# Performance work log

Measured on AMD Instinct MI355X. Metric: run time of the kernel, lower is better.

The kernel has to match this reference:

```python
import jax, jax.numpy as jnp
import numpy as np

N, E, IN_DIM, HID, L = 50000, 800000, 64, 64, 3
EDGE_DIM = 2 * HID + 2  # src_h | dst_h | edge_feat


def setup_inputs() -> dict:
    key = jax.random.key(0)
    ks = jax.random.split(key, 32)
    s = 0.05
    inp = {
        "h": jax.random.normal(ks[0], (N, IN_DIM), jnp.float32),
        "e": jax.random.normal(ks[1], (E, 2), jnp.float32),
        "src": jax.random.randint(ks[2], (E,), 0, N),
        "dst": jax.random.randint(ks[3], (E,), 0, N),
        # input embedding
        "emb_W": jax.random.normal(ks[4], (IN_DIM, HID), jnp.float32) * s,
        "emb_b": jnp.zeros((HID,), jnp.float32),
        # per-GIN-layer params (stacked over L)
        "eps": jnp.zeros((L,), jnp.float32),  # learn_eps init 0
        "mlp_W1": jax.random.normal(ks[5], (L, HID, HID), jnp.float32) * s,
        "mlp_b1": jnp.zeros((L, HID), jnp.float32),
        "mlp_bn_s": jnp.ones((L, HID), jnp.float32),   # eval-mode BN folded: x*s+sh
        "mlp_bn_sh": jnp.zeros((L, HID), jnp.float32),
        "mlp_W2": jax.random.normal(ks[6], (L, HID, HID), jnp.float32) * s,
        "mlp_b2": jnp.zeros((L, HID), jnp.float32),
        "apply_bn_s": jnp.ones((L, HID), jnp.float32),
        "apply_bn_sh": jnp.zeros((L, HID), jnp.float32),
        "gin_bn_s": jnp.ones((L, HID), jnp.float32),
        "gin_bn_sh": jnp.zeros((L, HID), jnp.float32),
        # prediction heads (L+1 of them)
        "pred_W1": jax.random.normal(ks[7], (L + 1, EDGE_DIM, HID), jnp.float32) * s,
        "pred_b1": jnp.zeros((L + 1, HID), jnp.float32),
        "pred_W2": jax.random.normal(ks[8], (L + 1, HID, 1), jnp.float32) * s,
        "pred_b2": jnp.zeros((L + 1, 1), jnp.float32),
    }
    return inp


def reference(h, e, src, dst, emb_W, emb_b, eps,
              mlp_W1, mlp_b1, mlp_bn_s, mlp_bn_sh, mlp_W2, mlp_b2,
              apply_bn_s, apply_bn_sh, gin_bn_s, gin_bn_sh,
              pred_W1, pred_b1, pred_W2, pred_b2):
    n = h.shape[0]
    bn = lambda x, sc, sh: x * sc + sh  # eval-mode batchnorm (folded scale/shift)

    h = h @ emb_W + emb_b  # [N, HID]

    def edge_feat(hh):
        # gather node features onto edges: [E, 2*HID+2]
        return jnp.concatenate([hh[src], hh[dst], e], axis=1)

    def pred(ef, i):
        z = jax.nn.relu(ef @ pred_W1[i] + pred_b1[i])
        return z @ pred_W2[i] + pred_b2[i]  # [E, 1]

    score = pred(edge_feat(h), 0)
    for i in range(L):
        h_in = h
        # GIN sum aggregation: copy src features, sum at dst
        neigh = jax.ops.segment_sum(h[src], dst, num_segments=n)
        x = (1.0 + eps[i]) * h + neigh
        # MLP: Linear -> BN -> ReLU -> Linear
        x = jax.nn.relu(bn(x @ mlp_W1[i] + mlp_b1[i], mlp_bn_s[i], mlp_bn_sh[i]))
        x = x @ mlp_W2[i] + mlp_b2[i]
        # ApplyNodeFunc: BN -> ReLU
        x = jax.nn.relu(bn(x, apply_bn_s[i], apply_bn_sh[i]))
        # GINLayer post: BN -> ReLU -> residual (dropout=0 in eval)
        x = jax.nn.relu(bn(x, gin_bn_s[i], gin_bn_sh[i]))
        h = h_in + x
        score = score + pred(edge_feat(h), i + 1)
    return jax.nn.relu(score)
```

## Files before the change

### kernel.cpp

```cpp
#include <hip/hip_runtime.h>

typedef unsigned short ushort_t;
typedef unsigned int uint_t;

static __device__ __forceinline__ ushort_t f2bf(float f) {
    uint_t u = __float_as_uint(f);
    uint_t r = (u + 0x7FFFu + ((u >> 16) & 1u)) >> 16;
    return (ushort_t)r;
}
static __device__ __forceinline__ float bf2f(ushort_t u) {
    return __uint_as_float(((uint_t)u) << 16);
}
static __device__ __forceinline__ float bf2f_lo(uint_t u) {
    return __uint_as_float(u << 16);
}
static __device__ __forceinline__ float bf2f_hi(uint_t u) {
    return __uint_as_float(u & 0xffff0000u);
}
static __device__ __forceinline__ uint_t pack2(float lo, float hi) {
    return (uint_t)f2bf(lo) | ((uint_t)f2bf(hi) << 16);
}

static __device__ __forceinline__ float edge_p2(
    uint_t ax, uint_t ay, float4 brow, float ex, float ey,
    float4 wc0, float4 wc1, float4 w2v)
{
    float z0 = bf2f_lo(ax) + brow.x + ex*wc0.x + ey*wc1.x; z0 = fmaxf(z0, 0.f);
    float z1 = bf2f_hi(ax) + brow.y + ex*wc0.y + ey*wc1.y; z1 = fmaxf(z1, 0.f);
    float z2 = bf2f_lo(ay) + brow.z + ex*wc0.z + ey*wc1.z; z2 = fmaxf(z2, 0.f);
    float z3 = bf2f_hi(ay) + brow.w + ex*wc0.w + ey*wc1.w; z3 = fmaxf(z3, 0.f);
    return z0*w2v.x + z1*w2v.y + z2*w2v.z + z3*w2v.w;
}

#define RED16(p) { p += __shfl_xor(p,1); p += __shfl_xor(p,2); \
                   p += __shfl_xor(p,4); p += __shfl_xor(p,8); }

__global__ __launch_bounds__(256) void k_count(
    const int* __restrict__ dst, int* __restrict__ deg, int E)
{
    int e = blockIdx.x * 256 + threadIdx.x;
    if (e < E) atomicAdd(&deg[dst[e]], 1);
}

__global__ __launch_bounds__(1024) void k_scanA(
    const int* __restrict__ deg, int* __restrict__ partial,
    int* __restrict__ bsum, int N)
{
    __shared__ int wsum[16];
    int tid = threadIdx.x, lane = tid & 63, wid = tid >> 6;
    int idx = blockIdx.x * 1024 + tid;
    int v = (idx < N) ? deg[idx] : 0;
    int x = v;
#pragma unroll
    for (int o = 1; o < 64; o <<= 1) {
        int t = __shfl_up(x, o, 64);
        if (lane >= o) x += t;
    }
    if (lane == 63) wsum[wid] = x;
    __syncthreads();
    if (wid == 0) {
        int s = (lane < 16) ? wsum[lane] : 0;
#pragma unroll
        for (int o = 1; o < 16; o <<= 1) {
            int t = __shfl_up(s, o, 64);
            if (lane >= o) s += t;
        }
        if (lane < 16) wsum[lane] = s;
    }
    __syncthreads();
    int woff = (wid > 0) ? wsum[wid - 1] : 0;
    if (idx < N) partial[idx] = woff + x - v;
    if (tid == 0) bsum[blockIdx.x] = wsum[15];
}

__global__ __launch_bounds__(256) void k_scanB(
    int* __restrict__ bsum, int nb, int* __restrict__ totalp)
{
    __shared__ int s[256];
    int tid = threadIdx.x;
    int v = (tid < nb) ? bsum[tid] : 0;
    s[tid] = v;
    __syncthreads();
#pragma unroll
    for (int off = 1; off < 256; off <<= 1) {
        int t = (tid >= off) ? s[tid - off] : 0;
        __syncthreads();
        s[tid] += t;
        __syncthreads();
    }
    if (tid < nb) bsum[tid] = s[tid] - v;
    if (tid == 0) totalp[0] = s[255];
}

__global__ __launch_bounds__(256) void k_scanC(
    int* __restrict__ offsets, const int* __restrict__ bsum,
    int* __restrict__ cursor, int N)
{
    int idx = blockIdx.x * 256 + threadIdx.x;
    if (idx >= N) return;
    int o = offsets[idx] + bsum[idx >> 10];
    offsets[idx] = o;
    cursor[idx] = o;
}

__global__ __launch_bounds__(256) void k_fill(
    const int* __restrict__ src, const int* __restrict__ dst,
    const float* __restrict__ ep, int* __restrict__ cursor,
    int4* __restrict__ entries, int E)
{
    int ei = blockIdx.x * 256 + threadIdx.x;
    if (ei >= E) return;
    int pos = atomicAdd(&cursor[dst[ei]], 1);
    float2 ev = *(const float2*)(ep + 2 * (size_t)ei);
    entries[pos] = make_int4(src[ei], ei, __float_as_int(ev.x), __float_as_int(ev.y));
}

static __device__ __forceinline__ int deg_bucket(int d) {
    return d >= 63 ? 0 : (63 - d);
}

__global__ __launch_bounds__(256) void k_bcount(
    const int* __restrict__ offsets, int* __restrict__ bcnt, int N)
{
    __shared__ int hist[64];
    int tid = threadIdx.x;
    if (tid < 64) hist[tid] = 0;
    __syncthreads();
    int idx = blockIdx.x * 256 + tid;
    if (idx < N) {
        int d = offsets[idx + 1] - offsets[idx];
        atomicAdd(&hist[deg_bucket(d)], 1);
    }
    __syncthreads();
    if (tid < 64 && hist[tid]) atomicAdd(&bcnt[tid], hist[tid]);
}

__global__ __launch_bounds__(64) void k_bscan(
    int* __restrict__ bcnt, int* __restrict__ bcur)
{
    int lane = threadIdx.x;
    int v = bcnt[lane];
    int x = v;
#pragma unroll
    for (int o = 1; o < 64; o <<= 1) {
        int t = __shfl_up(x, o, 64);
        if (lane >= o) x += t;
    }
    bcur[lane] = x - v;
}

__global__ __launch_bounds__(256) void k_bfill(
    const int* __restrict__ offsets, int* __restrict__ bcur,
    int* __restrict__ perm, int N)
{
    __shared__ int hist[64];
    __shared__ int lbase[64];
    int tid = threadIdx.x;
    if (tid < 64) hist[tid] = 0;
    __syncthreads();
    int idx = blockIdx.x * 256 + tid;
    int b = 0, rank = 0;
    bool valid = (idx < N);
    if (valid) {
        int d = offsets[idx + 1] - offsets[idx];
        b = deg_bucket(d);
        rank = atomicAdd(&hist[b], 1);
    }
    __syncthreads();
    if (tid < 64) lbase[tid] = hist[tid] ? atomicAdd(&bcur[tid], hist[tid]) : 0;
    __syncthreads();
    if (valid) perm[lbase[b] + rank] = idx;
}

template <int WRITE>
static __device__ __forceinline__ void epi_tables16(
    float (*xs)[68], int row16, int li, int r, float4 o,
    const float* __restrict__ WAn, const float* __restrict__ bAn,
    const float* __restrict__ WBn,
    ushort_t* __restrict__ tab_out, ushort_t* __restrict__ B_out)
{
    xs[row16][4*li+0] = o.x; xs[row16][4*li+1] = o.y;
    xs[row16][4*li+2] = o.z; xs[row16][4*li+3] = o.w;
    float4 aA = *(const float4*)(bAn + 4 * li);
    float4 aB = make_float4(0.f, 0.f, 0.f, 0.f);
#pragma unroll
    for (int k = 0; k < 64; k++) {
        float xk = xs[row16][k];
        float4 wa = *(const float4*)(WAn + k * 64 + 4 * li);
        float4 wb = *(const float4*)(WBn + k * 64 + 4 * li);
        aA.x += xk * wa.x; aA.y += xk * wa.y; aA.z += xk * wa.z; aA.w += xk * wa.w;
        aB.x += xk * wb.x; aB.y += xk * wb.y; aB.z += xk * wb.z; aB.w += xk * wb.w;
    }
    if (WRITE == 1) {
        int4 cw;
        cw.x = (int)pack2(aA.x, aA.y);
        cw.y = (int)pack2(aA.z, aA.w);
        cw.z = (int)pack2(o.x, o.y);
        cw.w = (int)pack2(o.z, o.w);
        *(int4*)(tab_out + (size_t)r * 128 + li * 8) = cw;
    } else {
        ushort4 oa;
        oa.x = f2bf(aA.x); oa.y = f2bf(aA.y); oa.z = f2bf(aA.z); oa.w = f2bf(aA.w);
        *(ushort4*)(tab_out + (size_t)r * 64 + 4 * li) = oa;
    }
    ushort4 ob;
    ob.x = f2bf(aB.x); ob.y = f2bf(aB.y); ob.z = f2bf(aB.z); ob.w = f2bf(aB.w);
    *(ushort4*)(B_out + (size_t)r * 64 + 4 * li) = ob;
}

__global__ __launch_bounds__(256) void k_embed_ab(
    const float* __restrict__ in, const float* __restrict__ W,
    const float* __restrict__ bias, float* __restrict__ hout,
    const float* __restrict__ WA, const float* __restrict__ bA,
    const float* __restrict__ WB,
    ushort_t* __restrict__ comb_out, ushort_t* __restrict__ B_out, int N)
{
    __shared__ float xs[16][68];
    const int row16 = threadIdx.x >> 4;
    const int li    = threadIdx.x & 15;
    const int r     = blockIdx.x * 16 + row16;
    if (r >= N) return;
    float4 x4 = *(const float4*)(in + (size_t)r * 64 + 4 * li);
    xs[row16][4*li+0] = x4.x; xs[row16][4*li+1] = x4.y;
    xs[row16][4*li+2] = x4.z; xs[row16][4*li+3] = x4.w;
    float4 acc = *(const float4*)(bias + 4 * li);
#pragma unroll
    for (int k = 0; k < 64; k++) {
        float xk = xs[row16][k];
        float4 wv = *(const float4*)(W + k * 64 + 4 * li);
        acc.x += xk * wv.x; acc.y += xk * wv.y;
        acc.z += xk * wv.z; acc.w += xk * wv.w;
    }
    *(float4*)(hout + (size_t)r * 64 + 4 * li) = acc;
    epi_tables16<1>(xs, row16, li, r, acc, WA, bA, WB, comb_out, B_out);
}

__global__ __launch_bounds__(256) void k_tables(
    const float* __restrict__ h,
    const float* __restrict__ WA, const float* __restrict__ bA,
    const float* __restrict__ WB,
    ushort_t* __restrict__ comb_out, ushort_t* __restrict__ B_out, int N)
{
    __shared__ float xs[16][68];
    const int row16 = threadIdx.x >> 4;
    const int li    = threadIdx.x & 15;
    const int r     = blockIdx.x * 16 + row16;
    if (r >= N) return;
    float4 o = *(const float4*)(h + (size_t)r * 64 + 4 * li);
    epi_tables16<1>(xs, row16, li, r, o, WA, bA, WB, comb_out, B_out);
}

template <int MODE, int EPI>
__global__ __launch_bounds__(256) void k_fused(
    const float* __restrict__ h, float* __restrict__ hout,
    const ushort_t* __restrict__ comb, const ushort_t* __restrict__ Bm,
    const int4* __restrict__ entries, const int* __restrict__ offsets,
    const int* __restrict__ perm,
    float* __restrict__ score_csr,
    const float* __restrict__ Wc, const float* __restrict__ W2v,
    const float* __restrict__ b2p, const float* __restrict__ epsp,
    const float* __restrict__ W1, const float* __restrict__ b1,
    const float* __restrict__ s1, const float* __restrict__ sh1,
    const float* __restrict__ W2, const float* __restrict__ b2,
    const float* __restrict__ as_, const float* __restrict__ ash,
    const float* __restrict__ gs, const float* __restrict__ gsh,
    const float* __restrict__ WAn, const float* __restrict__ bAn,
    const float* __restrict__ WBn,
    ushort_t* __restrict__ tab_out, ushort_t* __restrict__ B_out, int N)
{
    __shared__ float xs[16][68];
    __shared__ float ts[16][68];
    const int row16 = threadIdx.x >> 4;
    const int li    = threadIdx.x & 15;
    const int idx   = blockIdx.x * 16 + row16;
    if (idx >= N) return;
    const int r = perm[idx];

    const float4 wc0 = *(const float4*)(Wc + li*4);
    const float4 wc1 = *(const float4*)(Wc + 64 + li*4);
    const float4 w2v = *(const float4*)(W2v + li*4);
    const float bb2 = b2p[0];
    ushort4 bu = *(const ushort4*)(Bm + (size_t)r * 64 + li*4);
    const float4 brow = make_float4(bf2f(bu.x), bf2f(bu.y), bf2f(bu.z), bf2f(bu.w));

    const int beg = offsets[r], end = offsets[r + 1];
    float4 acc = make_float4(0.f, 0.f, 0.f, 0.f);

    for (int k = beg; k < end; k += 8) {
        int4 ee[8];
#pragma unroll
        for (int j = 0; j < 8; j++) {
            int kj = k + j; kj = kj < end ? kj : end - 1;
            ee[j] = entries[kj];
        }
        int4 cc[8];
#pragma unroll
        for (int j = 0; j < 8; j++)
            cc[j] = *(const int4*)(comb + (size_t)ee[j].x * 128 + li * 8);
#pragma unroll
        for (int j = 0; j < 8; j++) {
            const bool ok = (k + j < end);
            uint_t hz = ok ? (uint_t)cc[j].z : 0u;
            uint_t hw = ok ? (uint_t)cc[j].w : 0u;
            acc.x += bf2f_lo(hz); acc.y += bf2f_hi(hz);
            acc.z += bf2f_lo(hw); acc.w += bf2f_hi(hw);
        }
#pragma unroll
        for (int j = 0; j < 8; j++) {
            float p = edge_p2((uint_t)cc[j].x, (uint_t)cc[j].y, brow,
                              __int_as_float(ee[j].z), __int_as_float(ee[j].w),
                              wc0, wc1, w2v);
            RED16(p)
            if (li == 0 && (k + j < end)) {
                if (MODE == 0) score_csr[k + j] = p + bb2;
                else           score_csr[k + j] += p + bb2;
            }
        }
    }

    const float epsv = 1.0f + epsp[0];
    float4 hv = *(const float4*)(h + (size_t)r * 64 + 4 * li);
    xs[row16][4*li+0] = epsv * hv.x + acc.x;
    xs[row16][4*li+1] = epsv * hv.y + acc.y;
    xs[row16][4*li+2] = epsv * hv.z + acc.z;
    xs[row16][4*li+3] = epsv * hv.w + acc.w;

    float4 t = *(const float4*)(b1 + 4 * li);
#pragma unroll
    for (int kk = 0; kk < 64; kk++) {
        float xk = xs[row16][kk];
        float4 wv = *(const float4*)(W1 + kk * 64 + 4 * li);
        t.x += xk * wv.x; t.y += xk * wv.y; t.z += xk * wv.z; t.w += xk * wv.w;
    }
    {
        float4 sc = *(const float4*)(s1 + 4 * li);
        float4 sh = *(const float4*)(sh1 + 4 * li);
        t.x = fmaxf(t.x * sc.x + sh.x, 0.f);
        t.y = fmaxf(t.y * sc.y + sh.y, 0.f);
        t.z = fmaxf(t.z * sc.z + sh.z, 0.f);
        t.w = fmaxf(t.w * sc.w + sh.w, 0.f);
    }
    ts[row16][4*li+0] = t.x; ts[row16][4*li+1] = t.y;
    ts[row16][4*li+2] = t.z; ts[row16][4*li+3] = t.w;

    float4 u = *(const float4*)(b2 + 4 * li);
#pragma unroll
    for (int kk = 0; kk < 64; kk++) {
        float tk = ts[row16][kk];
        float4 wv = *(const float4*)(W2 + kk * 64 + 4 * li);
        u.x += tk * wv.x; u.y += tk * wv.y; u.z += tk * wv.z; u.w += tk * wv.w;
    }
    {
        float4 sc = *(const float4*)(as_ + 4 * li);
        float4 sh = *(const float4*)(ash + 4 * li);
        u.x = fmaxf(u.x * sc.x + sh.x, 0.f);
        u.y = fmaxf(u.y * sc.y + sh.y, 0.f);
        u.z = fmaxf(u.z * sc.z + sh.z, 0.f);
        u.w = fmaxf(u.w * sc.w + sh.w, 0.f);
        sc = *(const float4*)(gs + 4 * li);
        sh = *(const float4*)(gsh + 4 * li);
        u.x = fmaxf(u.x * sc.x + sh.x, 0.f);
        u.y = fmaxf(u.y * sc.y + sh.y, 0.f);
        u.z = fmaxf(u.z * sc.z + sh.z, 0.f);
        u.w = fmaxf(u.w * sc.w + sh.w, 0.f);
    }
    float4 o = make_float4(hv.x + u.x, hv.y + u.y, hv.z + u.z, hv.w + u.w);
    *(float4*)(hout + (size_t)r * 64 + 4 * li) = o;

    if (EPI == 1)
        epi_tables16<1>(xs, row16, li, r, o, WAn, bAn, WBn, tab_out, B_out);
    else if (EPI == 2)
        epi_tables16<2>(xs, row16, li, r, o, WAn, bAn, WBn, tab_out, B_out);
}

template <int COMPACT>
__global__ __launch_bounds__(256) void k_head(
    const ushort_t* __restrict__ Atab,
    const ushort_t* __restrict__ Bm,
    const int4* __restrict__ entries, const int* __restrict__ offsets,
    const int* __restrict__ perm,
    const float* __restrict__ score_csr, float* __restrict__ score_out,
    const float* __restrict__ Wc, const float* __restrict__ W2v,
    const float* __restrict__ b2p, int N)
{
    const int row16 = threadIdx.x >> 4;
    const int li    = threadIdx.x & 15;
    const int idx   = blockIdx.x * 16 + row16;
    if (idx >= N) return;
    const int r = perm[idx];

    const float4 wc0 = *(const float4*)(Wc + li*4);
    const float4 wc1 = *(const float4*)(Wc + 64 + li*4);
    const float4 w2v = *(const float4*)(W2v + li*4);
    const float bb2 = b2p[0];
    ushort4 bu = *(const ushort4*)(Bm + (size_t)r * 64 + li*4);
    const float4 brow = make_float4(bf2f(bu.x), bf2f(bu.y), bf2f(bu.z), bf2f(bu.w));

    const int beg = offsets[r], end = offsets[r + 1];

    for (int k = beg; k < end; k += 8) {
        int4 ee[8];
#pragma unroll
        for (int j = 0; j < 8; j++) {
            int kj = k + j; kj = kj < end ? kj : end - 1;
            ee[j] = entries[kj];
        }
        uint_t ax[8], ay[8];
#pragma unroll
        for (int j = 0; j < 8; j++) {
            if (COMPACT) {
                ushort4 a = *(const ushort4*)(Atab + (size_t)ee[j].x * 64 + li * 4);
                ax[j] = (uint_t)a.x | ((uint_t)a.y << 16);
                ay[j] = (uint_t)a.z | ((uint_t)a.w << 16);
            } else {
                int2 d = *(const int2*)(Atab + (size_t)ee[j].x * 128 + li * 8);
                ax[j] = (uint_t)d.x; ay[j] = (uint_t)d.y;
            }
        }
#pragma unroll
        for (int j = 0; j < 8; j++) {
            float p = edge_p2(ax[j], ay[j], brow,
                              __int_as_float(ee[j].z), __int_as_float(ee[j].w),
                              wc0, wc1, w2v);
            RED16(p)
            if (li == 0 && (k + j < end))
                score_out[ee[j].y] = fmaxf(score_csr[k + j] + p + bb2, 0.f);
        }
    }
}

extern "C" void kernel_launch(void* const* d_in, const int* in_sizes, int n_in,
                              void* d_out, int out_size, void* d_ws, size_t ws_size,
                              hipStream_t stream) {
    const float* h_in  = (const float*)d_in[0];
    const float* e     = (const float*)d_in[1];
    const int*   src   = (const int*)d_in[2];
    const int*   dst   = (const int*)d_in[3];
    const float* emb_W = (const float*)d_in[4];
    const float* emb_b = (const float*)d_in[5];
    const float* eps   = (const float*)d_in[6];
    const float* mW1   = (const float*)d_in[7];
    const float* mb1   = (const float*)d_in[8];
    const float* mbs   = (const float*)d_in[9];
    const float* mbsh  = (const float*)d_in[10];
    const float* mW2   = (const float*)d_in[11];
    const float* mb2   = (const float*)d_in[12];
    const float* as_   = (const float*)d_in[13];
    const float* ash   = (const float*)d_in[14];
    const float* gs    = (const float*)d_in[15];
    const float* gsh   = (const float*)d_in[16];
    const float* pW1   = (const float*)d_in[17];
    const float* pb1   = (const float*)d_in[18];
    const float* pW2   = (const float*)d_in[19];
    const float* pb2   = (const float*)d_in[20];

    const int N  = in_sizes[0] / 64;
    const int E  = in_sizes[2];
    const int Lr = in_sizes[6];
    const size_t nrow = (size_t)N * 64;

    float* score = (float*)d_out;

    char* wp = (char*)d_ws;
    auto take = [&](size_t b) -> char* {
        char* p = wp; wp += (b + 255) & ~(size_t)255; return p;
    };
    float*    h0        = (float*)take(nrow * 4);
    float*    h1        = (float*)take(nrow * 4);
    ushort_t* comb0     = (ushort_t*)take(nrow * 4);
    ushort_t* B0        = (ushort_t*)take(nrow * 2);
    int4*     entries   = (int4*)take((size_t)E * 16);
    float*    score_csr = (float*)take((size_t)E * 4);
    int*      offsets   = (int*)take((size_t)(N + 1) * 4);
    int*      cursor    = (int*)take((size_t)N * 4);
    int*      bsum      = (int*)take(1024);
    int*      perm      = (int*)take((size_t)N * 4);
    int*      bcnt      = (int*)take(64 * 4);
    int*      bcur      = (int*)take(64 * 4);
    ushort_t* comb1     = (ushort_t*)take(nrow * 4);
    ushort_t* B1        = (ushort_t*)take(nrow * 2);
    ushort_t* Afin      = (ushort_t*)take(nrow * 2);
    size_t need_epi = (size_t)(wp - (char*)d_ws);

    const bool use_epi = ws_size >= need_epi;

    const int rowBlocks = (N + 15) / 16;
    const int edgeGrid  = (E + 255) / 256;
    const int nb        = (N + 1023) / 1024;

    hipMemsetAsync(cursor, 0, (size_t)N * sizeof(int), stream);
    k_count<<<edgeGrid, 256, 0, stream>>>(dst, cursor, E);
    k_scanA<<<nb, 1024, 0, stream>>>(cursor, offsets, bsum, N);
    k_scanB<<<1, 256, 0, stream>>>(bsum, nb, offsets + N);
    k_scanC<<<(N + 255) / 256, 256, 0, stream>>>(offsets, bsum, cursor, N);
    k_fill<<<edgeGrid, 256, 0, stream>>>(src, dst, e, cursor, entries, E);

    hipMemsetAsync(bcnt, 0, 64 * sizeof(int), stream);
    k_bcount<<<(N + 255) / 256, 256, 0, stream>>>(offsets, bcnt, N);
    k_bscan<<<1, 64, 0, stream>>>(bcnt, bcur);
    k_bfill<<<(N + 255) / 256, 256, 0, stream>>>(offsets, bcur, perm, N);

    k_embed_ab<<<rowBlocks, 256, 0, stream>>>(
        h_in, emb_W, emb_b, h0, pW1, pb1, pW1 + 64 * 64, comb0, B0, N);

    float* hcur = h0;       float* hnext = h1;
    ushort_t* Ccur = comb0; ushort_t* Cnxt = use_epi ? comb1 : comb0;
    ushort_t* Bcur = B0;    ushort_t* Bnxt = use_epi ? B1 : B0;

    for (int i = 0; i < Lr; i++) {
        const float* pw  = pW1 + (size_t)i * 130 * 64;
        const float* Wc  = pw + 128 * 64;
        const float* w2  = pW2 + (size_t)i * 64;
        const float* b2  = pb2 + i;
        const float* pwn = pW1 + (size_t)(i + 1) * 130 * 64;
        const float* gW1 = mW1 + (size_t)i * 64 * 64;
        const float* gW2 = mW2 + (size_t)i * 64 * 64;
        const bool last = (i == Lr - 1);

        if (use_epi) {
            ushort_t* tout = last ? Afin : Cnxt;
            if (i == 0 && !last)
                k_fused<0,1><<<rowBlocks, 256, 0, stream>>>(
                    hcur, hnext, Ccur, Bcur, entries, offsets, perm, score_csr,
                    Wc, w2, b2, eps + i,
                    gW1, mb1 + i*64, mbs + i*64, mbsh + i*64, gW2, mb2 + i*64,
                    as_ + i*64, ash + i*64, gs + i*64, gsh + i*64,
                    pwn, pb1 + (i+1)*64, pwn + 64*64, tout, Bnxt, N);
            else if (i == 0 && last)
                k_fused<0,2><<<rowBlocks, 256, 0, stream>>>(
                    hcur, hnext, Ccur, Bcur, entries, offsets, perm, score_csr,
                    Wc, w2, b2, eps + i,
                    gW1, mb1 + i*64, mbs + i*64, mbsh + i*64, gW2, mb2 + i*64,
                    as_ + i*64, ash + i*64, gs + i*64, gsh + i*64,
                    pwn, pb1 + (i+1)*64, pwn + 64*64, tout, Bnxt, N);
            else if (!last)
                k_fused<1,1><<<rowBlocks, 256, 0, stream>>>(
                    hcur, hnext, Ccur, Bcur, entries, offsets, perm, score_csr,
                    Wc, w2, b2, eps + i,
                    gW1, mb1 + i*64, mbs + i*64, mbsh + i*64, gW2, mb2 + i*64,
                    as_ + i*64, ash + i*64, gs + i*64, gsh + i*64,
                    pwn, pb1 + (i+1)*64, pwn + 64*64, tout, Bnxt, N);
            else
                k_fused<1,2><<<rowBlocks, 256, 0, stream>>>(
                    hcur, hnext, Ccur, Bcur, entries, offsets, perm, score_csr,
                    Wc, w2, b2, eps + i,
                    gW1, mb1 + i*64, mbs + i*64, mbsh + i*64, gW2, mb2 + i*64,
                    as_ + i*64, ash + i*64, gs + i*64, gsh + i*64,
                    pwn, pb1 + (i+1)*64, pwn + 64*64, tout, Bnxt, N);
            { ushort_t* t = Ccur; Ccur = Cnxt; Cnxt = t; }
            { ushort_t* t = Bcur; Bcur = Bnxt; Bnxt = t; }
        } else {
            if (i == 0)
                k_fused<0,0><<<rowBlocks, 256, 0, stream>>>(
                    hcur, hnext, Ccur, Bcur, entries, offsets, perm, score_csr,
                    Wc, w2, b2, eps + i,
                    gW1, mb1 + i*64, mbs + i*64, mbsh + i*64, gW2, mb2 + i*64,
                    as_ + i*64, ash + i*64, gs + i*64, gsh + i*64,
                    nullptr, nullptr, nullptr, nullptr, nullptr, N);
            else
                k_fused<1,0><<<rowBlocks, 256, 0, stream>>>(
                    hcur, hnext, Ccur, Bcur, entries, offsets, perm, score_csr,
                    Wc, w2, b2, eps + i,
                    gW1, mb1 + i*64, mbs + i*64, mbsh + i*64, gW2, mb2 + i*64,
                    as_ + i*64, ash + i*64, gs + i*64, gsh + i*64,
                    nullptr, nullptr, nullptr, nullptr, nullptr, N);
            k_tables<<<rowBlocks, 256, 0, stream>>>(
                hnext, pwn, pb1 + (i+1)*64, pwn + 64*64, Ccur, Bcur, N);
        }
        { float* t = hcur; hcur = hnext; hnext = t; }
    }

    {
        const float* pw = pW1 + (size_t)Lr * 130 * 64;
        const float* Wc = pw + 128 * 64;
        const float* w2 = pW2 + (size_t)Lr * 64;
        const float* b2 = pb2 + Lr;
        if (use_epi)
            k_head<1><<<rowBlocks, 256, 0, stream>>>(
                Afin, Bcur, entries, offsets, perm, score_csr, score,
                Wc, w2, b2, N);
        else
            k_head<0><<<rowBlocks, 256, 0, stream>>>(
                Ccur, Bcur, entries, offsets, perm, score_csr, score,
                Wc, w2, b2, N);
    }
}
```

Measured before the change: 612.9 us.

## Process two nodes per 16-lane group and fold degree histogram into scan

The fused layer kernel now has each 16-lane group handle two degree-sorted nodes, interleaving their edge gathers four at a time so more independent memory loads are in flight. The per-node MLP and table epilogue move into a helper that runs twice, and the second shared buffer is dropped by reusing xs. The degree-bucket histogram is computed inside k_scanA, which removes the separate k_bcount launch, and the head kernel's edge loop switches from 8-wide clamped batches to 4-wide batches with a scalar tail. The trade-off is more registers per thread and half as many blocks, which could lower occupancy.

After: 1.432 ms. 134% more time.

```diff
diff --git a/kernel.cpp b/kernel.cpp
--- a/kernel.cpp
+++ b/kernel.cpp
@@ -42,14 +42,22 @@
     if (e < E) atomicAdd(&deg[dst[e]], 1);
 }
 
+static __device__ __forceinline__ int deg_bucket(int d) {
+    return d >= 63 ? 0 : (63 - d);
+}
+
 __global__ __launch_bounds__(1024) void k_scanA(
     const int* __restrict__ deg, int* __restrict__ partial,
-    int* __restrict__ bsum, int N)
+    int* __restrict__ bsum, int* __restrict__ bcnt, int N)
 {
     __shared__ int wsum[16];
+    __shared__ int hist[64];
     int tid = threadIdx.x, lane = tid & 63, wid = tid >> 6;
+    if (tid < 64) hist[tid] = 0;
+    __syncthreads();
     int idx = blockIdx.x * 1024 + tid;
     int v = (idx < N) ? deg[idx] : 0;
+    if (idx < N) atomicAdd(&hist[deg_bucket(v)], 1);
     int x = v;
 #pragma unroll
     for (int o = 1; o < 64; o <<= 1) {
@@ -71,6 +79,8 @@
     int woff = (wid > 0) ? wsum[wid - 1] : 0;
     if (idx < N) partial[idx] = woff + x - v;
     if (tid == 0) bsum[blockIdx.x] = wsum[15];
+    __syncthreads();
+    if (tid < 64 && hist[tid]) atomicAdd(&bcnt[tid], hist[tid]);
 }
 
 __global__ __launch_bounds__(256) void k_scanB(
@@ -113,26 +123,6 @@
     int pos = atomicAdd(&cursor[dst[ei]], 1);
     float2 ev = *(const float2*)(ep + 2 * (size_t)ei);
     entries[pos] = make_int4(src[ei], ei, __float_as_int(ev.x), __float_as_int(ev.y));
-}
-
-static __device__ __forceinline__ int deg_bucket(int d) {
-    return d >= 63 ? 0 : (63 - d);
-}
-
-__global__ __launch_bounds__(256) void k_bcount(
-    const int* __restrict__ offsets, int* __restrict__ bcnt, int N)
-{
-    __shared__ int hist[64];
-    int tid = threadIdx.x;
-    if (tid < 64) hist[tid] = 0;
-    __syncthreads();
-    int idx = blockIdx.x * 256 + tid;
-    if (idx < N) {
-        int d = offsets[idx + 1] - offsets[idx];
-        atomicAdd(&hist[deg_bucket(d)], 1);
-    }
-    __syncthreads();
-    if (tid < 64 && hist[tid]) atomicAdd(&bcnt[tid], hist[tid]);
 }
 
 __global__ __launch_bounds__(64) void k_bscan(
@@ -174,18 +164,18 @@
 
 template <int WRITE>
 static __device__ __forceinline__ void epi_tables16(
-    float (*xs)[68], int row16, int li, int r, float4 o,
+    float (*xs)[68], int row, int li, int r, float4 o,
     const float* __restrict__ WAn, const float* __restrict__ bAn,
     const float* __restrict__ WBn,
     ushort_t* __restrict__ tab_out, ushort_t* __restrict__ B_out)
 {
-    xs[row16][4*li+0] = o.x; xs[row16][4*li+1] = o.y;
-    xs[row16][4*li+2] = o.z; xs[row16][4*li+3] = o.w;
+    xs[row][4*li+0] = o.x; xs[row][4*li+1] = o.y;
+    xs[row][4*li+2] = o.z; xs[row][4*li+3] = o.w;
     float4 aA = *(const float4*)(bAn + 4 * li);
     float4 aB = make_float4(0.f, 0.f, 0.f, 0.f);
 #pragma unroll
     for (int k = 0; k < 64; k++) {
-        float xk = xs[row16][k];
+        float xk = xs[row][k];
         float4 wa = *(const float4*)(WAn + k * 64 + 4 * li);
         float4 wb = *(const float4*)(WBn + k * 64 + 4 * li);
         aA.x += xk * wa.x; aA.y += xk * wa.y; aA.z += xk * wa.z; aA.w += xk * wa.w;
@@ -208,6 +198,72 @@
     *(ushort4*)(B_out + (size_t)r * 64 + 4 * li) = ob;
 }
 
+template <int EPI>
+static __device__ __forceinline__ void node_mlp(
+    float (*xs)[68], int row, int li, int r, float4 acc, float epsv,
+    const float* __restrict__ h, float* __restrict__ hout,
+    const float* __restrict__ W1, const float* __restrict__ b1,
+    const float* __restrict__ s1, const float* __restrict__ sh1,
+    const float* __restrict__ W2, const float* __restrict__ b2,
+    const float* __restrict__ as_, const float* __restrict__ ash,
+    const float* __restrict__ gs, const float* __restrict__ gsh,
+    const float* __restrict__ WAn, const float* __restrict__ bAn,
+    const float* __restrict__ WBn,
+    ushort_t* __restrict__ tab_out, ushort_t* __restrict__ B_out)
+{
+    float4 hv = *(const float4*)(h + (size_t)r * 64 + 4 * li);
+    xs[row][4*li+0] = epsv * hv.x + acc.x;
+    xs[row][4*li+1] = epsv * hv.y + acc.y;
+    xs[row][4*li+2] = epsv * hv.z + acc.z;
+    xs[row][4*li+3] = epsv * hv.w + acc.w;
+
+    float4 t = *(const float4*)(b1 + 4 * li);
+#pragma unroll
+    for (int kk = 0; kk < 64; kk++) {
+        float xk = xs[row][kk];
+        float4 wv = *(const float4*)(W1 + kk * 64 + 4 * li);
+        t.x += xk * wv.x; t.y += xk * wv.y; t.z += xk * wv.z; t.w += xk * wv.w;
+    }
+    {
+        float4 sc = *(const float4*)(s1 + 4 * li);
+        float4 sh = *(const float4*)(sh1 + 4 * li);
+        t.x = fmaxf(t.x * sc.x + sh.x, 0.f);
+        t.y = fmaxf(t.y * sc.y + sh.y, 0.f);
+        t.z = fmaxf(t.z * sc.z + sh.z, 0.f);
+        t.w = fmaxf(t.w * sc.w + sh.w, 0.f);
+    }
+    xs[row][4*li+0] = t.x; xs[row][4*li+1] = t.y;
+    xs[row][4*li+2] = t.z; xs[row][4*li+3] = t.w;
+
+    float4 u = *(const float4*)(b2 + 4 * li);
+#pragma unroll
+    for (int kk = 0; kk < 64; kk++) {
+        float tk = xs[row][kk];
+        float4 wv = *(const float4*)(W2 + kk * 64 + 4 * li);
+        u.x += tk * wv.x; u.y += tk * wv.y; u.z += tk * wv.z; u.w += tk * wv.w;
+    }
+    {
+        float4 sc = *(const float4*)(as_ + 4 * li);
+        float4 sh = *(const float4*)(ash + 4 * li);
+        u.x = fmaxf(u.x * sc.x + sh.x, 0.f);
+        u.y = fmaxf(u.y * sc.y + sh.y, 0.f);
+        u.z = fmaxf(u.z * sc.z + sh.z, 0.f);
+        u.w = fmaxf(u.w * sc.w + sh.w, 0.f);
+        sc = *(const float4*)(gs + 4 * li);
+        sh = *(const float4*)(gsh + 4 * li);
+        u.x = fmaxf(u.x * sc.x + sh.x, 0.f);
+        u.y = fmaxf(u.y * sc.y + sh.y, 0.f);
+        u.z = fmaxf(u.z * sc.z + sh.z, 0.f);
+        u.w = fmaxf(u.w * sc.w + sh.w, 0.f);
+    }
+    float4 o = make_float4(hv.x + u.x, hv.y + u.y, hv.z + u.z, hv.w + u.w);
+    *(float4*)(hout + (size_t)r * 64 + 4 * li) = o;
+    if (EPI == 1)
+        epi_tables16<1>(xs, row, li, r, o, WAn, bAn, WBn, tab_out, B_out);
+    else if (EPI == 2)
+        epi_tables16<2>(xs, row, li, r, o, WAn, bAn, WBn, tab_out, B_out);
+}
+
 __global__ __launch_bounds__(256) void k_embed_ab(
     const float* __restrict__ in, const float* __restrict__ W,
     const float* __restrict__ bias, float* __restrict__ hout,
@@ -249,6 +305,15 @@
     float4 o = *(const float4*)(h + (size_t)r * 64 + 4 * li);
     epi_tables16<1>(xs, row16, li, r, o, WA, bA, WB, comb_out, B_out);
 }
+
+#define GATH(s) (*(const int4*)(comb + (size_t)(s) * 128 + li * 8))
+#define AGGC(acc, c) { acc.x += bf2f_lo((uint_t)(c).z); acc.y += bf2f_hi((uint_t)(c).z); \
+                       acc.z += bf2f_lo((uint_t)(c).w); acc.w += bf2f_hi((uint_t)(c).w); }
+#define SCOR(kk, e_, c_, brow_) { \
+    float p_ = edge_p2((uint_t)(c_).x, (uint_t)(c_).y, brow_, \
+                       __int_as_float((e_).z), __int_as_float((e_).w), wc0, wc1, w2v); \
+    RED16(p_) \
+    if (li == 0) { if (MODE == 0) score_csr[kk] = p_ + bb2; else score_csr[kk] += p_ + bb2; } }
 
 template <int MODE, int EPI>
 __global__ __launch_bounds__(256) void k_fused(
@@ -268,109 +333,80 @@
     const float* __restrict__ WBn,
     ushort_t* __restrict__ tab_out, ushort_t* __restrict__ B_out, int N)
 {
-    __shared__ float xs[16][68];
-    __shared__ float ts[16][68];
-    const int row16 = threadIdx.x >> 4;
-    const int li    = threadIdx.x & 15;
-    const int idx   = blockIdx.x * 16 + row16;
-    if (idx >= N) return;
-    const int r = perm[idx];
+    __shared__ float xs[32][68];
+    const int gq = threadIdx.x >> 4;
+    const int li = threadIdx.x & 15;
+    const int i0 = blockIdx.x * 32 + 2 * gq;
+    const int i1 = i0 + 1;
+    if (i0 >= N) return;
+    const int r0 = perm[i0];
+    const bool v1 = (i1 < N);
+    const int r1 = v1 ? perm[i1] : r0;
 
     const float4 wc0 = *(const float4*)(Wc + li*4);
     const float4 wc1 = *(const float4*)(Wc + 64 + li*4);
     const float4 w2v = *(const float4*)(W2v + li*4);
     const float bb2 = b2p[0];
-    ushort4 bu = *(const ushort4*)(Bm + (size_t)r * 64 + li*4);
-    const float4 brow = make_float4(bf2f(bu.x), bf2f(bu.y), bf2f(bu.z), bf2f(bu.w));
-
-    const int beg = offsets[r], end = offsets[r + 1];
-    float4 acc = make_float4(0.f, 0.f, 0.f, 0.f);
-
-    for (int k = beg; k < end; k += 8) {
-        int4 ee[8];
-#pragma unroll
-        for (int j = 0; j < 8; j++) {
-            int kj = k + j; kj = kj < end ? kj : end - 1;
-            ee[j] = entries[kj];
-        }
-        int4 cc[8];
-#pragma unroll
-        for (int j = 0; j < 8; j++)
-            cc[j] = *(const int4*)(comb + (size_t)ee[j].x * 128 + li * 8);
-#pragma unroll
-        for (int j = 0; j < 8; j++) {
-            const bool ok = (k + j < end);
-            uint_t hz = ok ? (uint_t)cc[j].z : 0u;
-            uint_t hw = ok ? (uint_t)cc[j].w : 0u;
-            acc.x += bf2f_lo(hz); acc.y += bf2f_hi(hz);
-            acc.z += bf2f_lo(hw); acc.w += bf2f_hi(hw);
-        }
-#pragma unroll
-        for (int j = 0; j < 8; j++) {
-            float p = edge_p2((uint_t)cc[j].x, (uint_t)cc[j].y, brow,
-                              __int_as_float(ee[j].z), __int_as_float(ee[j].w),
-                              wc0, wc1, w2v);
-            RED16(p)
-            if (li == 0 && (k + j < end)) {
-                if (MODE == 0) score_csr[k + j] = p + bb2;
-                else           score_csr[k + j] += p + bb2;
-            }
-        }
+    ushort4 bu0 = *(const ushort4*)(Bm + (size_t)r0 * 64 + li*4);
+    ushort4 bu1 = *(const ushort4*)(Bm + (size_t)r1 * 64 + li*4);
+    const float4 brow0 = make_float4(bf2f(bu0.x), bf2f(bu0.y), bf2f(bu0.z), bf2f(bu0.w));
+    const float4 brow1 = make_float4(bf2f(bu1.x), bf2f(bu1.y), bf2f(bu1.z), bf2f(bu1.w));
+
+    const int end0 = offsets[r0 + 1];
+    int k0 = offsets[r0];
+    int k1 = 0, end1 = 0;
+    if (v1) { k1 = offsets[r1]; end1 = offsets[r1 + 1]; }
+    float4 acc0 = make_float4(0.f, 0.f, 0.f, 0.f);
+    float4 acc1 = make_float4(0.f, 0.f, 0.f, 0.f);
+
+    while (k0 + 3 < end0 && k1 + 3 < end1) {
+        int4 a0 = entries[k0], a1 = entries[k0+1], a2 = entries[k0+2], a3 = entries[k0+3];
+        int4 f0 = entries[k1], f1 = entries[k1+1], f2 = entries[k1+2], f3 = entries[k1+3];
+        int4 ca0 = GATH(a0.x), ca1 = GATH(a1.x), ca2 = GATH(a2.x), ca3 = GATH(a3.x);
+        int4 cb0 = GATH(f0.x), cb1 = GATH(f1.x), cb2 = GATH(f2.x), cb3 = GATH(f3.x);
+        AGGC(acc0, ca0) AGGC(acc0, ca1) AGGC(acc0, ca2) AGGC(acc0, ca3)
+        AGGC(acc1, cb0) AGGC(acc1, cb1) AGGC(acc1, cb2) AGGC(acc1, cb3)
+        SCOR(k0, a0, ca0, brow0) SCOR(k0+1, a1, ca1, brow0)
+        SCOR(k0+2, a2, ca2, brow0) SCOR(k0+3, a3, ca3, brow0)
+        SCOR(k1, f0, cb0, brow1) SCOR(k1+1, f1, cb1, brow1)
+        SCOR(k1+2, f2, cb2, brow1) SCOR(k1+3, f3, cb3, brow1)
+        k0 += 4; k1 += 4;
+    }
+    for (; k0 + 3 < end0; k0 += 4) {
+        int4 a0 = entries[k0], a1 = entries[k0+1], a2 = entries[k0+2], a3 = entries[k0+3];
+        int4 ca0 = GATH(a0.x), ca1 = GATH(a1.x), ca2 = GATH(a2.x), ca3 = GATH(a3.x);
+        AGGC(acc0, ca0) AGGC(acc0, ca1) AGGC(acc0, ca2) AGGC(acc0, ca3)
+        SCOR(k0, a0, ca0, brow0) SCOR(k0+1, a1, ca1, brow0)
+        SCOR(k0+2, a2, ca2, brow0) SCOR(k0+3, a3, ca3, brow0)
+    }
+    for (; k0 < end0; k0++) {
+        int4 a0 = entries[k0];
+        int4 ca0 = GATH(a0.x);
+        AGGC(acc0, ca0)
+        SCOR(k0, a0, ca0, brow0)
+    }
+    for (; k1 + 3 < end1; k1 += 4) {
+        int4 f0 = entries[k1], f1 = entries[k1+1], f2 = entries[k1+2], f3 = entries[k1+3];
+        int4 cb0 = GATH(f0.x), cb1 = GATH(f1.x), cb2 = GATH(f2.x), cb3 = GATH(f3.x);
+        AGGC(acc1, cb0) AGGC(acc1, cb1) AGGC(acc1, cb2) AGGC(acc1, cb3)
+        SCOR(k1, f0, cb0, brow1) SCOR(k1+1, f1, cb1, brow1)
+        SCOR(k1+2, f2, cb2, brow1) SCOR(k1+3, f3, cb3, brow1)
+    }
+    for (; k1 < end1; k1++) {
+        int4 f0 = entries[k1];
+        int4 cb0 = GATH(f0.x);
+        AGGC(acc1, cb0)
+        SCOR(k1, f0, cb0, brow1)
     }
 
     const float epsv = 1.0f + epsp[0];
-    float4 hv = *(const float4*)(h + (size_t)r * 64 + 4 * li);
-    xs[row16][4*li+0] = epsv * hv.x + acc.x;
-    xs[row16][4*li+1] = epsv * hv.y + acc.y;
-    xs[row16][4*li+2] = epsv * hv.z + acc.z;
-    xs[row16][4*li+3] = epsv * hv.w + acc.w;
-
-    float4 t = *(const float4*)(b1 + 4 * li);
-#pragma unroll
-    for (int kk = 0; kk < 64; kk++) {
-        float xk = xs[row16][kk];
-        float4 wv = *(const float4*)(W1 + kk * 64 + 4 * li);
-        t.x += xk * wv.x; t.y += xk * wv.y; t.z += xk * wv.z; t.w += xk * wv.w;
-    }
-    {
-        float4 sc = *(const float4*)(s1 + 4 * li);
-        float4 sh = *(const float4*)(sh1 + 4 * li);
-        t.x = fmaxf(t.x * sc.x + sh.x, 0.f);
-        t.y = fmaxf(t.y * sc.y + sh.y, 0.f);
-        t.z = fmaxf(t.z * sc.z + sh.z, 0.f);
-        t.w = fmaxf(t.w * sc.w + sh.w, 0.f);
-    }
-    ts[row16][4*li+0] = t.x; ts[row16][4*li+1] = t.y;
-    ts[row16][4*li+2] = t.z; ts[row16][4*li+3] = t.w;
-
-    float4 u = *(const float4*)(b2 + 4 * li);
-#pragma unroll
-    for (int kk = 0; kk < 64; kk++) {
-        float tk = ts[row16][kk];
-        float4 wv = *(const float4*)(W2 + kk * 64 + 4 * li);
-        u.x += tk * wv.x; u.y += tk * wv.y; u.z += tk * wv.z; u.w += tk * wv.w;
-    }
-    {
-        float4 sc = *(const float4*)(as_ + 4 * li);
-        float4 sh = *(const float4*)(ash + 4 * li);
-        u.x = fmaxf(u.x * sc.x + sh.x, 0.f);
-        u.y = fmaxf(u.y * sc.y + sh.y, 0.f);
-        u.z = fmaxf(u.z * sc.z + sh.z, 0.f);
-        u.w = fmaxf(u.w * sc.w + sh.w, 0.f);
-        sc = *(const float4*)(gs + 4 * li);
-        sh = *(const float4*)(gsh + 4 * li);
-        u.x = fmaxf(u.x * sc.x + sh.x, 0.f);
-        u.y = fmaxf(u.y * sc.y + sh.y, 0.f);
-        u.z = fmaxf(u.z * sc.z + sh.z, 0.f);
-        u.w = fmaxf(u.w * sc.w + sh.w, 0.f);
-    }
-    float4 o = make_float4(hv.x + u.x, hv.y + u.y, hv.z + u.z, hv.w + u.w);
-    *(float4*)(hout + (size_t)r * 64 + 4 * li) = o;
-
-    if (EPI == 1)
-        epi_tables16<1>(xs, row16, li, r, o, WAn, bAn, WBn, tab_out, B_out);
-    else if (EPI == 2)
-        epi_tables16<2>(xs, row16, li, r, o, WAn, bAn, WBn, tab_out, B_out);
+    node_mlp<EPI>(xs, 2*gq, li, r0, acc0, epsv, h, hout,
+                  W1, b1, s1, sh1, W2, b2, as_, ash, gs, gsh,
+                  WAn, bAn, WBn, tab_out, B_out);
+    if (v1)
+        node_mlp<EPI>(xs, 2*gq+1, li, r1, acc1, epsv, h, hout,
+                      W1, b1, s1, sh1, W2, b2, as_, ash, gs, gsh,
+                      WAn, bAn, WBn, tab_out, B_out);
 }
 
 template <int COMPACT>
@@ -398,35 +434,38 @@
 
     const int beg = offsets[r], end = offsets[r + 1];
 
-    for (int k = beg; k < end; k += 8) {
-        int4 ee[8];
-#pragma unroll
-        for (int j = 0; j < 8; j++) {
-            int kj = k + j; kj = kj < end ? kj : end - 1;
-            ee[j] = entries[kj];
-        }
-        uint_t ax[8], ay[8];
-#pragma unroll
-        for (int j = 0; j < 8; j++) {
-            if (COMPACT) {
-                ushort4 a = *(const ushort4*)(Atab + (size_t)ee[j].x * 64 + li * 4);
-                ax[j] = (uint_t)a.x | ((uint_t)a.y << 16);
-                ay[j] = (uint_t)a.z | ((uint_t)a.w << 16);
-            } else {
-                int2 d = *(const int2*)(Atab + (size_t)ee[j].x * 128 + li * 8);
-                ax[j] = (uint_t)d.x; ay[j] = (uint_t)d.y;
-            }
-        }
-#pragma unroll
-        for (int j = 0; j < 8; j++) {
-            float p = edge_p2(ax[j], ay[j], brow,
-                              __int_as_float(ee[j].z), __int_as_float(ee[j].w),
-                              wc0, wc1, w2v);
-            RED16(p)
-            if (li == 0 && (k + j < end))
-                score_out[ee[j].y] = fmaxf(score_csr[k + j] + p + bb2, 0.f);
-        }
-    }
+#define ALOAD(s, ax, ay) { \
+    if (COMPACT) { \
+        ushort4 a_ = *(const ushort4*)(Atab + (size_t)(s) * 64 + li * 4); \
+        ax = (uint_t)a_.x | ((uint_t)a_.y << 16); \
+        ay = (uint_t)a_.z | ((uint_t)a_.w << 16); \
+    } else { \
+        int2 d_ = *(const int2*)(Atab + (size_t)(s) * 128 + li * 8); \
+        ax = (uint_t)d_.x; ay = (uint_t)d_.y; \
+    } }
+#define HSCOR(kk, e_, ax, ay) { \
+    float p_ = edge_p2(ax, ay, brow, __int_as_float((e_).z), __int_as_float((e_).w), \
+                       wc0, wc1, w2v); \
+    RED16(p_) \
+    if (li == 0) score_out[(e_).y] = fmaxf(score_csr[kk] + p_ + bb2, 0.f); }
+
+    int k = beg;
+    for (; k + 3 < end; k += 4) {
+        int4 e0 = entries[k], e1 = entries[k+1], e2 = entries[k+2], e3 = entries[k+3];
+        uint_t ax0, ay0, ax1, ay1, ax2, ay2, ax3, ay3;
+        ALOAD(e0.x, ax0, ay0) ALOAD(e1.x, ax1, ay1)
+        ALOAD(e2.x, ax2, ay2) ALOAD(e3.x, ax3, ay3)
+        HSCOR(k, e0, ax0, ay0) HSCOR(k+1, e1, ax1, ay1)
+        HSCOR(k+2, e2, ax2, ay2) HSCOR(k+3, e3, ax3, ay3)
+    }
+    for (; k < end; k++) {
+        int4 e0 = entries[k];
+        uint_t ax0, ay0;
+        ALOAD(e0.x, ax0, ay0)
+        HSCOR(k, e0, ax0, ay0)
+    }
+#undef ALOAD
+#undef HSCOR
 }
 
 extern "C" void kernel_launch(void* const* d_in, const int* in_sizes, int n_in,
@@ -484,19 +523,19 @@
 
     const bool use_epi = ws_size >= need_epi;
 
-    const int rowBlocks = (N + 15) / 16;
-    const int edgeGrid  = (E + 255) / 256;
-    const int nb        = (N + 1023) / 1024;
+    const int rowBlocks  = (N + 15) / 16;
+    const int dualBlocks = (N + 31) / 32;
+    const int edgeGrid   = (E + 255) / 256;
+    const int nb         = (N + 1023) / 1024;
 
     hipMemsetAsync(cursor, 0, (size_t)N * sizeof(int), stream);
+    hipMemsetAsync(bcnt, 0, 64 * sizeof(int), stream);
     k_count<<<edgeGrid, 256, 0, stream>>>(dst, cursor, E);
-    k_scanA<<<nb, 1024, 0, stream>>>(cursor, offsets, bsum, N);
+    k_scanA<<<nb, 1024, 0, stream>>>(cursor, offsets, bsum, bcnt, N);
     k_scanB<<<1, 256, 0, stream>>>(bsum, nb, offsets + N);
     k_scanC<<<(N + 255) / 256, 256, 0, stream>>>(offsets, bsum, cursor, N);
     k_fill<<<edgeGrid, 256, 0, stream>>>(src, dst, e, cursor, entries, E);
 
-    hipMemsetAsync(bcnt, 0, 64 * sizeof(int), stream);
-    k_bcount<<<(N + 255) / 256, 256, 0, stream>>>(offsets, bcnt, N);
     k_bscan<<<1, 64, 0, stream>>>(bcnt, bcur);
     k_bfill<<<(N + 255) / 256, 256, 0, stream>>>(offsets, bcur, perm, N);
 
@@ -520,28 +559,28 @@
         if (use_epi) {
             ushort_t* tout = last ? Afin : Cnxt;
             if (i == 0 && !last)
-                k_fused<0,1><<<rowBlocks, 256, 0, stream>>>(
+                k_fused<0,1><<<dualBlocks, 256, 0, stream>>>(
                     hcur, hnext, Ccur, Bcur, entries, offsets, perm, score_csr,
                     Wc, w2, b2, eps + i,
                     gW1, mb1 + i*64, mbs + i*64, mbsh + i*64, gW2, mb2 + i*64,
                     as_ + i*64, ash + i*64, gs + i*64, gsh + i*64,
                     pwn, pb1 + (i+1)*64, pwn + 64*64, tout, Bnxt, N);
             else if (i == 0 && last)
-                k_fused<0,2><<<rowBlocks, 256, 0, stream>>>(
+                k_fused<0,2><<<dualBlocks, 256, 0, stream>>>(
                     hcur, hnext, Ccur, Bcur, entries, offsets, perm, score_csr,
                     Wc, w2, b2, eps + i,
                     gW1, mb1 + i*64, mbs + i*64, mbsh + i*64, gW2, mb2 + i*64,
                     as_ + i*64, ash + i*64, gs + i*64, gsh + i*64,
                     pwn, pb1 + (i+1)*64, pwn + 64*64, tout, Bnxt, N);
             else if (!last)
-                k_fused<1,1><<<rowBlocks, 256, 0, stream>>>(
+                k_fused<1,1><<<dualBlocks, 256, 0, stream>>>(
                     hcur, hnext, Ccur, Bcur, entries, offsets, perm, score_csr,
                     Wc, w2, b2, eps + i,
                     gW1, mb1 + i*64, mbs + i*64, mbsh + i*64, gW2, mb2 + i*64,
                     as_ + i*64, ash + i*64, gs + i*64, gsh + i*64,
                     pwn, pb1 + (i+1)*64, pwn + 64*64, tout, Bnxt, N);
             else
-                k_fused<1,2><<<rowBlocks, 256, 0, stream>>>(
+                k_fused<1,2><<<dualBlocks, 256, 0, stream>>>(
                     hcur, hnext, Ccur, Bcur, entries, offsets, perm, score_csr,
                     Wc, w2, b2, eps + i,
                     gW1, mb1 + i*64, mbs + i*64, mbsh + i*64, gW2, mb2 + i*64,
@@ -551,14 +590,14 @@
             { ushort_t* t = Bcur; Bcur = Bnxt; Bnxt = t; }
         } else {
             if (i == 0)
-                k_fused<0,0><<<rowBlocks, 256, 0, stream>>>(
+                k_fused<0,0><<<dualBlocks, 256, 0, stream>>>(
                     hcur, hnext, Ccur, Bcur, entries, offsets, perm, score_csr,
                     Wc, w2, b2, eps + i,
                     gW1, mb1 + i*64, mbs + i*64, mbsh + i*64, gW2, mb2 + i*64,
                     as_ + i*64, ash + i*64, gs + i*64, gsh + i*64,
                     nullptr, nullptr, nullptr, nullptr, nullptr, N);
             else
-                k_fused<1,0><<<rowBlocks, 256, 0, stream>>>(
+                k_fused<1,0><<<dualBlocks, 256, 0, stream>>>(
                     hcur, hnext, Ccur, Bcur, entries, offsets, perm, score_csr,
                     Wc, w2, b2, eps + i,
                     gW1, mb1 + i*64, mbs + i*64, mbsh + i*64, gW2, mb2 + i*64,
```
